# Performance work log

Hardware: AMD Instinct MI355X
Metric: run time of the kernel (lower is better)

Reference implementation:

```python
import jax, jax.numpy as jnp
import numpy as np

B = 4096
OBS_DIM = 1024
E_OUT = 512
H1 = 2048
H2 = 2048


def setup_inputs() -> dict:
    key = jax.random.key(0)
    ks = jax.random.split(key, 12)
    def kaiming(k, shape, fan_in):
        return jax.random.normal(k, shape, dtype=jnp.float32) * np.float32(np.sqrt(2.0 / fan_in))
    obs = jax.random.normal(ks[0], (B, OBS_DIM), dtype=jnp.float32)
    # lineare: Linear(obs_dim, e_outputs), torch weight shape [out, in]
    We = kaiming(ks[1], (E_OUT, OBS_DIM), OBS_DIM)
    be = jax.random.normal(ks[2], (E_OUT,), dtype=jnp.float32) * 0.01
    # obs_dim attention heads, each Linear(e_outputs, 2), stacked
    attn_W = kaiming(ks[3], (OBS_DIM, E_OUT, 2), E_OUT)
    attn_b = jax.random.normal(ks[4], (OBS_DIM, 2), dtype=jnp.float32) * 0.01
    # v_net: Linear(obs_dim,H1)+tanh, Linear(H1,H2)+[dropout(eval:no-op)]+tanh, Linear(H2,1)
    W1 = kaiming(ks[5], (H1, OBS_DIM), OBS_DIM)
    b1 = jnp.zeros((H1,), dtype=jnp.float32)
    W2 = kaiming(ks[6], (H2, H1), H1)
    b2 = jnp.zeros((H2,), dtype=jnp.float32)
    W3 = kaiming(ks[7], (1, H2), H2)
    b3 = jnp.zeros((1,), dtype=jnp.float32)
    return {"obs": obs, "We": We, "be": be, "attn_W": attn_W, "attn_b": attn_b,
            "W1": W1, "b1": b1, "W2": W2, "b2": b2, "W3": W3, "b3": b3}


def reference(obs, We, be, attn_W, attn_b, W1, b1, W2, b2, W3, b3):
    # e = tanh(lineare(obs)) : [B, E_OUT]
    e = jnp.tanh(obs @ We.T + be)
    # all obs_dim attention heads batched into one contraction: [B, OBS_DIM, 2]
    logits = jnp.einsum('be,oec->boc', e, attn_W) + attn_b
    # softmax over the 2 logits, keep prob of class 1 -> Attention [B, OBS_DIM]
    attention = jax.nn.softmax(logits, axis=-1)[..., 1]
    state_attention = obs * attention
    # v_net (eval mode: dropout is identity)
    h = jnp.tanh(state_attention @ W1.T + b1)
    h = jnp.tanh(h @ W2.T + b2)
    v = jnp.squeeze(h @ W3.T + b3, -1)  # [B]
    return (v, attention)
```

## Files before the change

kernel.cpp:

```cpp
#include <hip/hip_runtime.h>
#include <hip/hip_bf16.h>

typedef unsigned short u16;
typedef u16 u16x4 __attribute__((ext_vector_type(4)));
typedef u16 u16x8 __attribute__((ext_vector_type(8)));
typedef __bf16 bf16x8 __attribute__((ext_vector_type(8)));
typedef float f32x4 __attribute__((ext_vector_type(4)));

__device__ __forceinline__ u16 f2bf(float f) {
  unsigned u = __float_as_uint(f);
  u += 0x7FFFu + ((u >> 16) & 1u);
  return (u16)(u >> 16);
}
__device__ __forceinline__ float bf2f(u16 h) {
  return __uint_as_float(((unsigned)h) << 16);
}
__device__ __forceinline__ float tanh_fast(float x) {
  float t = __expf(2.0f * x);
  return 1.0f - 2.0f / (t + 1.0f);
}
__device__ __forceinline__ float sigmoid_fast(float x) {
  return 1.0f / (1.0f + __expf(-x));
}

__device__ __forceinline__ void cvt4(const float* __restrict__ s, u16* __restrict__ d, int q) {
  float4 v = ((const float4*)s)[q];
  u16x4 o = { f2bf(v.x), f2bf(v.y), f2bf(v.z), f2bf(v.w) };
  ((u16x4*)d)[q] = o;
}

__global__ __launch_bounds__(256)
void prep_kernel(const float* __restrict__ obs, const float* __restrict__ We,
                 const float* __restrict__ W1, const float* __restrict__ W2,
                 const float* __restrict__ aW, const float* __restrict__ ab,
                 u16* __restrict__ obs_b, u16* __restrict__ We_b,
                 u16* __restrict__ W1_b, u16* __restrict__ W2_b,
                 u16* __restrict__ Wd, float* __restrict__ bd) {
  int q = blockIdx.x * 256 + threadIdx.x;
  if (q < 1048576) { cvt4(obs, obs_b, q); return; }
  q -= 1048576;
  if (q < 131072) { cvt4(We, We_b, q); return; }
  q -= 131072;
  if (q < 524288) { cvt4(W1, W1_b, q); return; }
  q -= 524288;
  if (q < 1048576) { cvt4(W2, W2_b, q); return; }
  q -= 1048576;
  if (q < 131072) {
    int i0 = q * 4;
    int o = i0 >> 9, e0 = i0 & 511;
    const float* p = aW + (size_t)o * 1024 + e0 * 2;
    float4 v0 = *(const float4*)p;
    float4 v1 = *(const float4*)(p + 4);
    u16x4 od = { f2bf(v0.y - v0.x), f2bf(v0.w - v0.z),
                 f2bf(v1.y - v1.x), f2bf(v1.w - v1.z) };
    *(u16x4*)(Wd + i0) = od;
    if (q < 256) {
      float4 a0 = *(const float4*)(ab + q * 8);
      float4 a1 = *(const float4*)(ab + q * 8 + 4);
      float4 ob = { a0.y - a0.x, a0.w - a0.z, a1.y - a1.x, a1.w - a1.z };
      *(float4*)(bd + q * 4) = ob;
    }
  }
}

template <int BM, int BN, int EP>
__global__ __launch_bounds__(256)
void gemm_bt(const u16* __restrict__ A, const u16* __restrict__ Bt,
             int N, int K,
             const float* __restrict__ bias,
             u16* __restrict__ outb, float* __restrict__ outf,
             const float* __restrict__ obs, u16* __restrict__ sa,
             const float* __restrict__ W3, const float* __restrict__ b3,
             float* __restrict__ vout) {
  constexpr int CA = BM / 64;
  constexpr int CB = BN / 64;
  constexpr int MI = BM / 32;
  constexpr int NJ = BN / 32;

  __shared__ __align__(16) u16 As[BM * 32];
  __shared__ __align__(16) u16 Bs[BN * 32];

  const int tid = threadIdx.x;
  const int lane = tid & 63;
  const int wave = tid >> 6;
  const int bm = blockIdx.x, bn = blockIdx.y;

  const int sr = tid >> 2;
  const int c0 = (tid & 3) * 8;

  const u16* gA[CA];
  const u16* gB[CB];
#pragma unroll
  for (int q = 0; q < CA; ++q)
    gA[q] = A + (size_t)(bm * BM + sr + q * 64) * K + c0;
#pragma unroll
  for (int q = 0; q < CB; ++q)
    gB[q] = Bt + (size_t)(bn * BN + sr + q * 64) * K + c0;

  u16x8 pa[CA], pb[CB];
#pragma unroll
  for (int q = 0; q < CA; ++q) { pa[q] = *(const u16x8*)gA[q]; gA[q] += 32; }
#pragma unroll
  for (int q = 0; q < CB; ++q) { pb[q] = *(const u16x8*)gB[q]; gB[q] += 32; }

  const int wm = (wave >> 1) * (BM / 2);
  const int wn = (wave & 1) * (BN / 2);
  const int fr = lane & 15;
  const int koff = (lane >> 4) * 8;

  f32x4 acc[MI][NJ];
#pragma unroll
  for (int i = 0; i < MI; ++i)
#pragma unroll
    for (int j = 0; j < NJ; ++j)
      acc[i][j] = (f32x4){0.f, 0.f, 0.f, 0.f};

  const int T = K >> 5;
  for (int k = 0; k < T; ++k) {
    __syncthreads();
#pragma unroll
    for (int q = 0; q < CA; ++q) *(u16x8*)(As + (sr + q * 64) * 32 + c0) = pa[q];
#pragma unroll
    for (int q = 0; q < CB; ++q) *(u16x8*)(Bs + (sr + q * 64) * 32 + c0) = pb[q];
    __syncthreads();

    if (k + 1 < T) {
#pragma unroll
      for (int q = 0; q < CA; ++q) { pa[q] = *(const u16x8*)gA[q]; gA[q] += 32; }
#pragma unroll
      for (int q = 0; q < CB; ++q) { pb[q] = *(const u16x8*)gB[q]; gB[q] += 32; }
    }

    bf16x8 a[MI], b[NJ];
#pragma unroll
    for (int i = 0; i < MI; ++i)
      a[i] = *(const bf16x8*)(As + (wm + i * 16 + fr) * 32 + koff);
#pragma unroll
    for (int j = 0; j < NJ; ++j)
      b[j] = *(const bf16x8*)(Bs + (wn + j * 16 + fr) * 32 + koff);
#pragma unroll
    for (int i = 0; i < MI; ++i)
#pragma unroll
      for (int j = 0; j < NJ; ++j)
        acc[i][j] = __builtin_amdgcn_mfma_f32_16x16x32_bf16(a[i], b[j], acc[i][j], 0, 0, 0);
  }

  if constexpr (EP == 2) {
    float vpart[MI][4];
#pragma unroll
    for (int i = 0; i < MI; ++i)
#pragma unroll
      for (int r = 0; r < 4; ++r) vpart[i][r] = 0.f;
#pragma unroll
    for (int j = 0; j < NJ; ++j) {
      const int col = bn * BN + wn + j * 16 + fr;
      const float bv = bias[col];
      const float w3 = W3[col];
#pragma unroll
      for (int i = 0; i < MI; ++i)
#pragma unroll
        for (int r = 0; r < 4; ++r)
          vpart[i][r] += tanh_fast(acc[i][j][r] + bv) * w3;
    }
    const bool lead = (fr == 0);
    const bool addb = (bn == 0) && ((wave & 1) == 0);
#pragma unroll
    for (int i = 0; i < MI; ++i)
#pragma unroll
      for (int r = 0; r < 4; ++r) {
        float p = vpart[i][r];
        p += __shfl_xor(p, 8);
        p += __shfl_xor(p, 4);
        p += __shfl_xor(p, 2);
        p += __shfl_xor(p, 1);
        if (lead) {
          const int row = bm * BM + wm + i * 16 + (lane >> 4) * 4 + r;
          atomicAdd(vout + row, addb ? p + b3[0] : p);
        }
      }
  } else {
#pragma unroll
    for (int j = 0; j < NJ; ++j) {
      const int col = bn * BN + wn + j * 16 + fr;
      const float bv = bias[col];
#pragma unroll
      for (int i = 0; i < MI; ++i) {
#pragma unroll
        for (int r = 0; r < 4; ++r) {
          const int row = bm * BM + wm + i * 16 + (lane >> 4) * 4 + r;
          const float x = acc[i][j][r] + bv;
          const size_t idx = (size_t)row * N + col;
          if constexpr (EP == 0) {
            outb[idx] = f2bf(tanh_fast(x));
          } else {
            const float att = sigmoid_fast(x);
            outf[idx] = att;
            sa[idx] = f2bf(obs[idx] * att);
          }
        }
      }
    }
  }
}

extern "C" void kernel_launch(void* const* d_in, const int* in_sizes, int n_in,
                              void* d_out, int out_size, void* d_ws, size_t ws_size,
                              hipStream_t stream) {
  const float* obs   = (const float*)d_in[0];
  const float* We    = (const float*)d_in[1];
  const float* be    = (const float*)d_in[2];
  const float* attnW = (const float*)d_in[3];
  const float* attnb = (const float*)d_in[4];
  const float* W1    = (const float*)d_in[5];
  const float* b1    = (const float*)d_in[6];
  const float* W2    = (const float*)d_in[7];
  const float* b2    = (const float*)d_in[8];
  const float* W3    = (const float*)d_in[9];
  const float* b3    = (const float*)d_in[10];
  float* out = (float*)d_out;

  char* ws = (char*)d_ws;
  u16*   We_b  = (u16*)(ws + 0x00000000);
  u16*   Wd_b  = (u16*)(ws + 0x00100000);
  u16*   W1_b  = (u16*)(ws + 0x00200000);
  u16*   W2_b  = (u16*)(ws + 0x00600000);
  float* bd    = (float*)(ws + 0x00E00000);
  u16*   obs_b = (u16*)(ws + 0x00E01000);
  u16*   e_b   = (u16*)(ws + 0x01601000);
  u16*   sa_b  = (u16*)(ws + 0x01A01000);
  u16*   h1_b  = (u16*)(ws + 0x02201000);

  hipMemsetAsync(out, 0, 4096 * sizeof(float), stream);

  prep_kernel<<<11264, 256, 0, stream>>>(obs, We, W1, W2, attnW, attnb,
                                         obs_b, We_b, W1_b, W2_b, Wd_b, bd);

  gemm_bt<128, 64, 0><<<dim3(32, 8), 256, 0, stream>>>(
      obs_b, We_b, 512, 1024, be, e_b, nullptr, nullptr, nullptr, nullptr, nullptr, nullptr);
  gemm_bt<128, 64, 1><<<dim3(32, 16), 256, 0, stream>>>(
      e_b, Wd_b, 1024, 512, bd, nullptr, out + 4096, obs, sa_b, nullptr, nullptr, nullptr);
  gemm_bt<128, 128, 0><<<dim3(32, 16), 256, 0, stream>>>(
      sa_b, W1_b, 2048, 1024, b1, h1_b, nullptr, nullptr, nullptr, nullptr, nullptr, nullptr);
  gemm_bt<128, 128, 2><<<dim3(32, 16), 256, 0, stream>>>(
      h1_b, W2_b, 2048, 2048, b2, nullptr, nullptr, nullptr, nullptr, W3, b3, out);
}
```

Measured before the change: 217.1 us.

## Fuse prep and four GEMMs into one persistent kernel with grid barriers

```diff
diff --git a/kernel.cpp b/kernel.cpp
--- a/kernel.cpp
+++ b/kernel.cpp
@@ -12,9 +12,6 @@
   u += 0x7FFFu + ((u >> 16) & 1u);
   return (u16)(u >> 16);
 }
-__device__ __forceinline__ float bf2f(u16 h) {
-  return __uint_as_float(((unsigned)h) << 16);
-}
 __device__ __forceinline__ float tanh_fast(float x) {
   float t = __expf(2.0f * x);
   return 1.0f - 2.0f / (t + 1.0f);
@@ -22,69 +19,41 @@
 __device__ __forceinline__ float sigmoid_fast(float x) {
   return 1.0f / (1.0f + __expf(-x));
 }
-
 __device__ __forceinline__ void cvt4(const float* __restrict__ s, u16* __restrict__ d, int q) {
   float4 v = ((const float4*)s)[q];
   u16x4 o = { f2bf(v.x), f2bf(v.y), f2bf(v.z), f2bf(v.w) };
   ((u16x4*)d)[q] = o;
 }
 
-__global__ __launch_bounds__(256)
-void prep_kernel(const float* __restrict__ obs, const float* __restrict__ We,
-                 const float* __restrict__ W1, const float* __restrict__ W2,
-                 const float* __restrict__ aW, const float* __restrict__ ab,
-                 u16* __restrict__ obs_b, u16* __restrict__ We_b,
-                 u16* __restrict__ W1_b, u16* __restrict__ W2_b,
-                 u16* __restrict__ Wd, float* __restrict__ bd) {
-  int q = blockIdx.x * 256 + threadIdx.x;
-  if (q < 1048576) { cvt4(obs, obs_b, q); return; }
-  q -= 1048576;
-  if (q < 131072) { cvt4(We, We_b, q); return; }
-  q -= 131072;
-  if (q < 524288) { cvt4(W1, W1_b, q); return; }
-  q -= 524288;
-  if (q < 1048576) { cvt4(W2, W2_b, q); return; }
-  q -= 1048576;
-  if (q < 131072) {
-    int i0 = q * 4;
-    int o = i0 >> 9, e0 = i0 & 511;
-    const float* p = aW + (size_t)o * 1024 + e0 * 2;
-    float4 v0 = *(const float4*)p;
-    float4 v1 = *(const float4*)(p + 4);
-    u16x4 od = { f2bf(v0.y - v0.x), f2bf(v0.w - v0.z),
-                 f2bf(v1.y - v1.x), f2bf(v1.w - v1.z) };
-    *(u16x4*)(Wd + i0) = od;
-    if (q < 256) {
-      float4 a0 = *(const float4*)(ab + q * 8);
-      float4 a1 = *(const float4*)(ab + q * 8 + 4);
-      float4 ob = { a0.y - a0.x, a0.w - a0.z, a1.y - a1.x, a1.w - a1.z };
-      *(float4*)(bd + q * 4) = ob;
-    }
-  }
+__device__ __forceinline__ void grid_barrier(unsigned int* cnt, unsigned int target) {
+  __syncthreads();
+  if (threadIdx.x == 0) {
+    __threadfence();
+    atomicAdd(cnt, 1u);
+    while (atomicAdd(cnt, 0u) < target)
+      __builtin_amdgcn_s_sleep(8);
+    __threadfence();
+  }
+  __syncthreads();
 }
 
 template <int BM, int BN, int EP>
-__global__ __launch_bounds__(256)
-void gemm_bt(const u16* __restrict__ A, const u16* __restrict__ Bt,
-             int N, int K,
-             const float* __restrict__ bias,
-             u16* __restrict__ outb, float* __restrict__ outf,
-             const float* __restrict__ obs, u16* __restrict__ sa,
-             const float* __restrict__ W3, const float* __restrict__ b3,
-             float* __restrict__ vout) {
+__device__ __forceinline__ void gemm_tile(
+    const u16* __restrict__ A, const u16* __restrict__ Bt,
+    int N, int K, const float* __restrict__ bias,
+    u16* __restrict__ outb, float* __restrict__ outf,
+    const float* __restrict__ obs, u16* __restrict__ sa,
+    const float* __restrict__ W3, const float* __restrict__ b3,
+    float* __restrict__ vout,
+    u16* As, u16* Bs, int bm, int bn) {
   constexpr int CA = BM / 64;
   constexpr int CB = BN / 64;
   constexpr int MI = BM / 32;
   constexpr int NJ = BN / 32;
 
-  __shared__ __align__(16) u16 As[BM * 32];
-  __shared__ __align__(16) u16 Bs[BN * 32];
-
   const int tid = threadIdx.x;
   const int lane = tid & 63;
   const int wave = tid >> 6;
-  const int bm = blockIdx.x, bn = blockIdx.y;
-
   const int sr = tid >> 2;
   const int c0 = (tid & 3) * 8;
 
@@ -201,6 +170,71 @@
       }
     }
   }
+}
+
+__global__ __launch_bounds__(256, 2)
+void mega(const float* __restrict__ obs, const float* __restrict__ We,
+          const float* __restrict__ be, const float* __restrict__ attnW,
+          const float* __restrict__ attnb,
+          const float* __restrict__ W1, const float* __restrict__ b1,
+          const float* __restrict__ W2, const float* __restrict__ b2,
+          const float* __restrict__ W3, const float* __restrict__ b3,
+          float* __restrict__ out,
+          u16* __restrict__ We_b, u16* __restrict__ Wd,
+          u16* __restrict__ W1_b, u16* __restrict__ W2_b,
+          float* __restrict__ bd, u16* __restrict__ obs_b,
+          u16* __restrict__ e_b, u16* __restrict__ sa_b,
+          u16* __restrict__ h1_b, unsigned int* __restrict__ bar) {
+  __shared__ __align__(16) u16 As[128 * 32];
+  __shared__ __align__(16) u16 Bs[128 * 32];
+
+  const int gtid = blockIdx.x * 256 + threadIdx.x;
+  const int b = blockIdx.x;
+
+  if (gtid < 1024) ((float4*)out)[gtid] = (float4){0.f, 0.f, 0.f, 0.f};
+  for (int q0 = gtid; q0 < 2883584; q0 += 131072) {
+    int q = q0;
+    if (q < 1048576) { cvt4(obs, obs_b, q); continue; }
+    q -= 1048576;
+    if (q < 131072) { cvt4(We, We_b, q); continue; }
+    q -= 131072;
+    if (q < 524288) { cvt4(W1, W1_b, q); continue; }
+    q -= 524288;
+    if (q < 1048576) { cvt4(W2, W2_b, q); continue; }
+    q -= 1048576;
+    {
+      int i0 = q * 4;
+      int o = i0 >> 9, e0 = i0 & 511;
+      const float* p = attnW + (size_t)o * 1024 + e0 * 2;
+      float4 v0 = *(const float4*)p;
+      float4 v1 = *(const float4*)(p + 4);
+      u16x4 od = { f2bf(v0.y - v0.x), f2bf(v0.w - v0.z),
+                   f2bf(v1.y - v1.x), f2bf(v1.w - v1.z) };
+      *(u16x4*)(Wd + i0) = od;
+      if (q < 256) {
+        float4 a0 = *(const float4*)(attnb + q * 8);
+        float4 a1 = *(const float4*)(attnb + q * 8 + 4);
+        float4 ob = { a0.y - a0.x, a0.w - a0.z, a1.y - a1.x, a1.w - a1.z };
+        *(float4*)(bd + q * 4) = ob;
+      }
+    }
+  }
+  grid_barrier(bar + 0, 512);
+
+  gemm_tile<64, 64, 0>(obs_b, We_b, 512, 1024, be, e_b, nullptr, nullptr,
+                       nullptr, nullptr, nullptr, nullptr, As, Bs, b >> 3, b & 7);
+  grid_barrier(bar + 1, 512);
+
+  gemm_tile<128, 64, 1>(e_b, Wd, 1024, 512, bd, nullptr, out + 4096, obs,
+                        sa_b, nullptr, nullptr, nullptr, As, Bs, b >> 4, b & 15);
+  grid_barrier(bar + 2, 512);
+
+  gemm_tile<128, 128, 0>(sa_b, W1_b, 2048, 1024, b1, h1_b, nullptr, nullptr,
+                         nullptr, nullptr, nullptr, nullptr, As, Bs, b >> 4, b & 15);
+  grid_barrier(bar + 3, 512);
+
+  gemm_tile<128, 128, 2>(h1_b, W2_b, 2048, 2048, b2, nullptr, nullptr, nullptr,
+                         nullptr, W3, b3, out, As, Bs, b >> 4, b & 15);
 }
 
 extern "C" void kernel_launch(void* const* d_in, const int* in_sizes, int n_in,
@@ -229,18 +263,11 @@
   u16*   e_b   = (u16*)(ws + 0x01601000);
   u16*   sa_b  = (u16*)(ws + 0x01A01000);
   u16*   h1_b  = (u16*)(ws + 0x02201000);
-
-  hipMemsetAsync(out, 0, 4096 * sizeof(float), stream);
-
-  prep_kernel<<<11264, 256, 0, stream>>>(obs, We, W1, W2, attnW, attnb,
-                                         obs_b, We_b, W1_b, W2_b, Wd_b, bd);
-
-  gemm_bt<128, 64, 0><<<dim3(32, 8), 256, 0, stream>>>(
-      obs_b, We_b, 512, 1024, be, e_b, nullptr, nullptr, nullptr, nullptr, nullptr, nullptr);
-  gemm_bt<128, 64, 1><<<dim3(32, 16), 256, 0, stream>>>(
-      e_b, Wd_b, 1024, 512, bd, nullptr, out + 4096, obs, sa_b, nullptr, nullptr, nullptr);
-  gemm_bt<128, 128, 0><<<dim3(32, 16), 256, 0, stream>>>(
-      sa_b, W1_b, 2048, 1024, b1, h1_b, nullptr, nullptr, nullptr, nullptr, nullptr, nullptr);
-  gemm_bt<128, 128, 2><<<dim3(32, 16), 256, 0, stream>>>(
-      h1_b, W2_b, 2048, 2048, b2, nullptr, nullptr, nullptr, nullptr, W3, b3, out);
-}
+  unsigned int* bar = (unsigned int*)(ws + 0x03201000);
+
+  hipMemsetAsync(bar, 0, 4 * sizeof(unsigned int), stream);
+
+  mega<<<512, 256, 0, stream>>>(obs, We, be, attnW, attnb, W1, b1, W2, b2,
+                                W3, b3, out, We_b, Wd_b, W1_b, W2_b, bd,
+                                obs_b, e_b, sa_b, h1_b, bar);
+}
```

Measured after the change: 461.5 us. 2.13x slower.

## Deepen GEMM K-tile to 64 with padded LDS rows and fold memset into prep

Applied to the files above, without the earlier changes.

```diff
diff --git a/kernel.cpp b/kernel.cpp
--- a/kernel.cpp
+++ b/kernel.cpp
@@ -35,8 +35,10 @@
                  const float* __restrict__ aW, const float* __restrict__ ab,
                  u16* __restrict__ obs_b, u16* __restrict__ We_b,
                  u16* __restrict__ W1_b, u16* __restrict__ W2_b,
-                 u16* __restrict__ Wd, float* __restrict__ bd) {
+                 u16* __restrict__ Wd, float* __restrict__ bd,
+                 float* __restrict__ vzero) {
   int q = blockIdx.x * 256 + threadIdx.x;
+  if (q < 1024) ((float4*)vzero)[q] = (float4){0.f, 0.f, 0.f, 0.f};
   if (q < 1048576) { cvt4(obs, obs_b, q); return; }
   q -= 1048576;
   if (q < 131072) { cvt4(We, We_b, q); return; }
@@ -64,44 +66,45 @@
 }
 
 template <int BM, int BN, int EP>
-__global__ __launch_bounds__(256)
+__global__ __launch_bounds__(256, 2)
 void gemm_bt(const u16* __restrict__ A, const u16* __restrict__ Bt,
              int N, int K,
              const float* __restrict__ bias,
              u16* __restrict__ outb, float* __restrict__ outf,
-             const float* __restrict__ obs, u16* __restrict__ sa,
+             const u16* __restrict__ obsb, u16* __restrict__ sa,
              const float* __restrict__ W3, const float* __restrict__ b3,
              float* __restrict__ vout) {
-  constexpr int CA = BM / 64;
-  constexpr int CB = BN / 64;
+  constexpr int LS = 72;
+  constexpr int CA = BM / 32;
+  constexpr int CB = BN / 32;
   constexpr int MI = BM / 32;
   constexpr int NJ = BN / 32;
 
-  __shared__ __align__(16) u16 As[BM * 32];
-  __shared__ __align__(16) u16 Bs[BN * 32];
+  __shared__ __align__(16) u16 As[BM * LS];
+  __shared__ __align__(16) u16 Bs[BN * LS];
 
   const int tid = threadIdx.x;
   const int lane = tid & 63;
   const int wave = tid >> 6;
   const int bm = blockIdx.x, bn = blockIdx.y;
 
-  const int sr = tid >> 2;
-  const int c0 = (tid & 3) * 8;
+  const int r0 = tid >> 3;
+  const int kc = (tid & 7) * 8;
 
   const u16* gA[CA];
   const u16* gB[CB];
 #pragma unroll
   for (int q = 0; q < CA; ++q)
-    gA[q] = A + (size_t)(bm * BM + sr + q * 64) * K + c0;
+    gA[q] = A + (size_t)(bm * BM + r0 + q * 32) * K + kc;
 #pragma unroll
   for (int q = 0; q < CB; ++q)
-    gB[q] = Bt + (size_t)(bn * BN + sr + q * 64) * K + c0;
+    gB[q] = Bt + (size_t)(bn * BN + r0 + q * 32) * K + kc;
 
   u16x8 pa[CA], pb[CB];
 #pragma unroll
-  for (int q = 0; q < CA; ++q) { pa[q] = *(const u16x8*)gA[q]; gA[q] += 32; }
-#pragma unroll
-  for (int q = 0; q < CB; ++q) { pb[q] = *(const u16x8*)gB[q]; gB[q] += 32; }
+  for (int q = 0; q < CA; ++q) { pa[q] = *(const u16x8*)gA[q]; gA[q] += 64; }
+#pragma unroll
+  for (int q = 0; q < CB; ++q) { pb[q] = *(const u16x8*)gB[q]; gB[q] += 64; }
 
   const int wm = (wave >> 1) * (BM / 2);
   const int wn = (wave & 1) * (BN / 2);
@@ -115,34 +118,37 @@
     for (int j = 0; j < NJ; ++j)
       acc[i][j] = (f32x4){0.f, 0.f, 0.f, 0.f};
 
-  const int T = K >> 5;
+  const int T = K >> 6;
   for (int k = 0; k < T; ++k) {
     __syncthreads();
 #pragma unroll
-    for (int q = 0; q < CA; ++q) *(u16x8*)(As + (sr + q * 64) * 32 + c0) = pa[q];
-#pragma unroll
-    for (int q = 0; q < CB; ++q) *(u16x8*)(Bs + (sr + q * 64) * 32 + c0) = pb[q];
+    for (int q = 0; q < CA; ++q) *(u16x8*)(As + (r0 + q * 32) * LS + kc) = pa[q];
+#pragma unroll
+    for (int q = 0; q < CB; ++q) *(u16x8*)(Bs + (r0 + q * 32) * LS + kc) = pb[q];
     __syncthreads();
 
     if (k + 1 < T) {
 #pragma unroll
-      for (int q = 0; q < CA; ++q) { pa[q] = *(const u16x8*)gA[q]; gA[q] += 32; }
-#pragma unroll
-      for (int q = 0; q < CB; ++q) { pb[q] = *(const u16x8*)gB[q]; gB[q] += 32; }
-    }
-
-    bf16x8 a[MI], b[NJ];
-#pragma unroll
-    for (int i = 0; i < MI; ++i)
-      a[i] = *(const bf16x8*)(As + (wm + i * 16 + fr) * 32 + koff);
-#pragma unroll
-    for (int j = 0; j < NJ; ++j)
-      b[j] = *(const bf16x8*)(Bs + (wn + j * 16 + fr) * 32 + koff);
-#pragma unroll
-    for (int i = 0; i < MI; ++i)
+      for (int q = 0; q < CA; ++q) { pa[q] = *(const u16x8*)gA[q]; gA[q] += 64; }
+#pragma unroll
+      for (int q = 0; q < CB; ++q) { pb[q] = *(const u16x8*)gB[q]; gB[q] += 64; }
+    }
+
+#pragma unroll
+    for (int s = 0; s < 2; ++s) {
+      bf16x8 a[MI], b[NJ];
+#pragma unroll
+      for (int i = 0; i < MI; ++i)
+        a[i] = *(const bf16x8*)(As + (wm + i * 16 + fr) * LS + s * 32 + koff);
 #pragma unroll
       for (int j = 0; j < NJ; ++j)
-        acc[i][j] = __builtin_amdgcn_mfma_f32_16x16x32_bf16(a[i], b[j], acc[i][j], 0, 0, 0);
+        b[j] = *(const bf16x8*)(Bs + (wn + j * 16 + fr) * LS + s * 32 + koff);
+#pragma unroll
+      for (int i = 0; i < MI; ++i)
+#pragma unroll
+        for (int j = 0; j < NJ; ++j)
+          acc[i][j] = __builtin_amdgcn_mfma_f32_16x16x32_bf16(a[i], b[j], acc[i][j], 0, 0, 0);
+    }
   }
 
   if constexpr (EP == 2) {
@@ -195,7 +201,7 @@
           } else {
             const float att = sigmoid_fast(x);
             outf[idx] = att;
-            sa[idx] = f2bf(obs[idx] * att);
+            sa[idx] = f2bf(bf2f(obsb[idx]) * att);
           }
         }
       }
@@ -230,15 +236,13 @@
   u16*   sa_b  = (u16*)(ws + 0x01A01000);
   u16*   h1_b  = (u16*)(ws + 0x02201000);
 
-  hipMemsetAsync(out, 0, 4096 * sizeof(float), stream);
-
   prep_kernel<<<11264, 256, 0, stream>>>(obs, We, W1, W2, attnW, attnb,
-                                         obs_b, We_b, W1_b, W2_b, Wd_b, bd);
-
-  gemm_bt<128, 64, 0><<<dim3(32, 8), 256, 0, stream>>>(
+                                         obs_b, We_b, W1_b, W2_b, Wd_b, bd, out);
+
+  gemm_bt<64, 64, 0><<<dim3(64, 8), 256, 0, stream>>>(
       obs_b, We_b, 512, 1024, be, e_b, nullptr, nullptr, nullptr, nullptr, nullptr, nullptr);
   gemm_bt<128, 64, 1><<<dim3(32, 16), 256, 0, stream>>>(
-      e_b, Wd_b, 1024, 512, bd, nullptr, out + 4096, obs, sa_b, nullptr, nullptr, nullptr);
+      e_b, Wd_b, 1024, 512, bd, nullptr, out + 4096, obs_b, sa_b, nullptr, nullptr, nullptr);
   gemm_bt<128, 128, 0><<<dim3(32, 16), 256, 0, stream>>>(
       sa_b, W1_b, 2048, 1024, b1, h1_b, nullptr, nullptr, nullptr, nullptr, nullptr, nullptr);
   gemm_bt<128, 128, 2><<<dim3(32, 16), 256, 0, stream>>>(
```

Result: faster. 205.8 us (-5.2%).
